# Kernel optimization log

Measured on AMD Instinct MI355X. Metric: run time of the kernel, lower is better.

Reference implementation:

```python
import jax, jax.numpy as jnp
import numpy as np

EMBED = 1024
HEADS = 16
HEAD_DIM = EMBED // HEADS
RANK = 8
ALPHA = 16
SCALE_LORA = ALPHA / RANK  # 2.0


def _lora_linear(x, W, b, A, B):
    # F.linear(x, W, b) + scale * F.linear(F.linear(x, A), B)
    return x @ W.T + b + SCALE_LORA * ((x @ A.T) @ B.T)


def setup_inputs() -> dict:
    key = jax.random.key(0)
    ks = jax.random.split(key, 17)
    d = {"x": jax.random.normal(ks[0], (2, 2048, EMBED), dtype=jnp.float32)}
    names = ["q", "k", "v", "o"]
    i = 1
    for n in names:
        d[f"W{n}"] = jax.random.normal(ks[i], (EMBED, EMBED), dtype=jnp.float32) * 0.02; i += 1
        d[f"b{n}"] = jnp.zeros((EMBED,), dtype=jnp.float32)
        d[f"A{n}"] = jax.random.normal(ks[i], (RANK, EMBED), dtype=jnp.float32) * 0.02; i += 1
        d[f"B{n}"] = jax.random.normal(ks[i], (EMBED, RANK), dtype=jnp.float32) * 0.02; i += 1
    return d


def reference(x, Wq, bq, Aq, Bq, Wk, bk, Ak, Bk, Wv, bv, Av, Bv, Wo, bo, Ao, Bo):
    N, S, _ = x.shape
    Q = _lora_linear(x, Wq, bq, Aq, Bq).reshape(N, S, HEADS, HEAD_DIM)
    K = _lora_linear(x, Wk, bk, Ak, Bk).reshape(N, S, HEADS, HEAD_DIM)
    V = _lora_linear(x, Wv, bv, Av, Bv).reshape(N, S, HEADS, HEAD_DIM)
    # energy: [N, H, Sq, Sk]
    energy = jnp.einsum("nqhd,nkhd->nhqk", Q, K) / jnp.sqrt(jnp.float32(HEAD_DIM))
    attn = jax.nn.softmax(energy, axis=-1)
    out = jnp.einsum("nhqk,nkhd->nqhd", attn, V).reshape(N, S, EMBED)
    return _lora_linear(out, Wo, bo, Ao, Bo)
```

## Files before the change

kernel.cpp:

```cpp
#include <hip/hip_runtime.h>
#include <stdint.h>

typedef uint16_t u16;
typedef short s16x8 __attribute__((ext_vector_type(8)));
typedef float f32x4 __attribute__((ext_vector_type(4)));
typedef unsigned short u16x4 __attribute__((ext_vector_type(4)));
typedef uint32_t u32;
typedef u32 u32x2 __attribute__((ext_vector_type(2)));
typedef u32 u32x4 __attribute__((ext_vector_type(4)));

#define MFMA16(a,b,c) __builtin_amdgcn_mfma_f32_16x16x32_bf16((a),(b),(c),0,0,0)
#define QSCALE 0.18033688011112042f

__device__ __forceinline__ float b2f(u16 b){
  union { u32 u; float f; } v; v.u = ((u32)b)<<16; return v.f;
}
__device__ __forceinline__ u16 f2b(float f){
  union { float f; u32 u; } v; v.f = f;
  return (u16)((v.u + 0x7fffu + ((v.u>>16)&1u))>>16);
}
__device__ __forceinline__ u32 fbits(float f){
  union { float f; u32 u; } v; v.f = f; return v.u;
}
__device__ __forceinline__ void load_lds_16B(const void* g, void* l){
  __builtin_amdgcn_global_load_lds((const __attribute__((address_space(1))) void*)g,
                                   (__attribute__((address_space(3))) void*)l, 16, 0, 0);
}

__global__ __launch_bounds__(256) void conv_kernel(
    const float* __restrict__ x, u16* __restrict__ xb,
    const float* __restrict__ W0, const float* __restrict__ W1,
    const float* __restrict__ W2, const float* __restrict__ W3,
    u16* __restrict__ Wb,
    const float* __restrict__ A0, const float* __restrict__ A1,
    const float* __restrict__ A2, const float* __restrict__ A3,
    u16* __restrict__ Abf)
{
  const int bid = blockIdx.x;
  if (bid < 1024){
    const int g = bid*256 + threadIdx.x;
#pragma unroll
    for (int t=0;t<4;t++){
      const int i4 = g + t*262144;
      const f32x4 v = *(const f32x4*)(x + (size_t)i4*4);
      u16x4 o;
#pragma unroll
      for (int j=0;j<4;j++) o[j] = f2b(v[j]);
      *(u16x4*)(xb + (size_t)i4*4) = o;
    }
    return;
  }
  if (bid < 2048){
    const int cv = bid - 1024;
    const int y = cv>>8;
    const float* src = (y==0)?W0:(y==1)?W1:(y==2)?W2:W3;
    u16* dst = Wb + (size_t)y*1048576;
    const int g = (cv&255)*256 + threadIdx.x;
#pragma unroll
    for (int t=0;t<4;t++){
      const int i4 = g + t*65536;
      const f32x4 v = *(const f32x4*)(src + (size_t)i4*4);
      u16x4 o;
#pragma unroll
      for (int j=0;j<4;j++) o[j] = f2b(v[j]);
      *(u16x4*)(dst + (size_t)i4*4) = o;
    }
    return;
  }
  for (int w = threadIdx.x; w < 8192; w += 256){
    const int proj = w >> 11, rem = w & 2047;
    const int row = rem >> 7, c8 = (rem & 127) << 3;
    u16x4 o0 = u16x4{0,0,0,0}, o1 = u16x4{0,0,0,0};
    if (row < 8){
      const float* ap = ((proj==0)?A0:(proj==1)?A1:(proj==2)?A2:A3) + row*1024 + c8;
      const f32x4 v0 = *(const f32x4*)(ap);
      const f32x4 v1 = *(const f32x4*)(ap+4);
#pragma unroll
      for (int j=0;j<4;j++){ o0[j] = f2b(v0[j]); o1[j] = f2b(v1[j]); }
    }
    u16* dp = Abf + (size_t)(proj*16 + row)*1024 + c8;
    *(u16x4*)(dp)   = o0;
    *(u16x4*)(dp+4) = o1;
  }
}

__global__ __launch_bounds__(256,2) void gemm_qkv_kernel(
    const u16* __restrict__ Xb, const u16* __restrict__ Wb,
    const float* __restrict__ bq, const float* __restrict__ bk, const float* __restrict__ bv,
    const u16* __restrict__ Abf,
    const float* __restrict__ Blq, const float* __restrict__ Blk, const float* __restrict__ Blv,
    u16* __restrict__ Qb, u16* __restrict__ Kb, u16* __restrict__ Vtb)
{
  __shared__ u16 sm[16896];
  u16* AtB = sm;
  u16* BtB = sm + 8192;
  const int tid = threadIdx.x;
  const int wid = tid>>6, lane = tid&63;
  const int quad = lane>>4, l16 = lane&15;
  const int wm = wid>>1, wn = wid&1;
  const int proj = blockIdx.x>>3;
  const int n0 = (blockIdx.x&7)<<7, m0 = blockIdx.y<<7;
  const u16* W = Wb + (size_t)proj*1048576;
  const u16* AbP = Abf + (size_t)proj*16384;
  const float* bias = (proj==0)?bq:(proj==1)?bk:bv;
  const float* Bl   = (proj==0)?Blq:(proj==1)?Blk:Blv;
  const float scale = (proj==0)?QSCALE:1.0f;

  f32x4 acc[4][4];
  f32x4 acc_t[4];
#pragma unroll
  for (int i=0;i<4;i++){
#pragma unroll
    for (int j=0;j<4;j++) acc[i][j] = f32x4{0.f,0.f,0.f,0.f};
    acc_t[i] = f32x4{0.f,0.f,0.f,0.f};
  }

  for (int k0=0;k0<1024;k0+=64){
#pragma unroll
    for (int half=0; half<2; half++){
#pragma unroll
      for (int p=0;p<2;p++){
        const int s = wid*128 + p*64 + lane;
        const int row = s>>2, c = s&3;
        load_lds_16B(Xb + (size_t)(m0+row)*1024 + k0 + half*32 + c*8, AtB + half*4096 + (wid*128+p*64)*8);
        load_lds_16B(W  + (size_t)(n0+row)*1024 + k0 + half*32 + c*8, BtB + half*4096 + (wid*128+p*64)*8);
      }
    }
    __syncthreads();
#pragma unroll
    for (int half=0; half<2; half++){
      s16x8 af[4], bfr[4];
#pragma unroll
      for (int t=0;t<4;t++){
        const int r = wm*64 + t*16 + l16;
        af[t]  = *(const s16x8*)(AtB + half*4096 + r*32 + quad*8);
        const int c = wn*64 + t*16 + l16;
        bfr[t] = *(const s16x8*)(BtB + half*4096 + c*32 + quad*8);
      }
      const s16x8 abf = *(const s16x8*)(AbP + (size_t)l16*1024 + k0 + half*32 + quad*8);
#pragma unroll
      for (int tm=0;tm<4;tm++){
#pragma unroll
        for (int tn=0;tn<4;tn++)
          acc[tm][tn] = MFMA16(af[tm], bfr[tn], acc[tm][tn]);
        acc_t[tm] = MFMA16(af[tm], abf, acc_t[tm]);
      }
    }
    __syncthreads();
  }

  float* tT = (float*)sm;
  if (wn==0 && l16<8){
#pragma unroll
    for (int tm=0;tm<4;tm++)
#pragma unroll
      for (int rg=0;rg<4;rg++)
        tT[(wm*64 + tm*16 + quad*4 + rg)*8 + l16] = acc_t[tm][rg];
  }
  __syncthreads();

  s16x8 tf[4], bfl[4];
#pragma unroll
  for (int t=0;t<4;t++){ tf[t] = s16x8{0,0,0,0,0,0,0,0}; bfl[t] = s16x8{0,0,0,0,0,0,0,0}; }
  if (quad==0){
#pragma unroll
    for (int tm=0;tm<4;tm++){
      const float* tp = tT + (wm*64 + tm*16 + l16)*8;
#pragma unroll
      for (int j=0;j<8;j++) tf[tm][j] = (short)f2b(2.0f*tp[j]);
    }
#pragma unroll
    for (int tn=0;tn<4;tn++){
      const float* bp = Bl + (size_t)(n0 + wn*64 + tn*16 + l16)*8;
      const f32x4 b0 = *(const f32x4*)(bp);
      const f32x4 b1 = *(const f32x4*)(bp+4);
#pragma unroll
      for (int j=0;j<4;j++){ bfl[tn][j] = (short)f2b(b0[j]); bfl[tn][4+j] = (short)f2b(b1[j]); }
    }
  }
#pragma unroll
  for (int tm=0;tm<4;tm++)
#pragma unroll
    for (int tn=0;tn<4;tn++)
      acc[tm][tn] = MFMA16(tf[tm], bfl[tn], acc[tm][tn]);

  if (proj==2){
    __syncthreads();
#pragma unroll
    for (int tn=0;tn<4;tn++){
      const int nl = wn*64 + tn*16 + l16;
      const float bn = bias[n0+nl];
#pragma unroll
      for (int tm=0;tm<4;tm++){
        const int ml = wm*64 + tm*16 + quad*4;
        u16x4 pk;
#pragma unroll
        for (int rg=0;rg<4;rg++) pk[rg] = f2b(acc[tm][tn][rg]+bn);
        *(u16x4*)(sm + nl*132 + ml) = pk;
      }
    }
    __syncthreads();
    const int batch = m0>>11, sbase = m0&2047;
#pragma unroll
    for (int p=0;p<8;p++){
      const int idx = p*256 + tid;
      const int row = idx>>4, c16 = idx&15;
      const s16x8 v = *(const s16x8*)(sm + row*132 + c16*8);
      const int ng = n0 + row, hh = ng>>6, dd = ng&63;
      *(s16x8*)(Vtb + (size_t)((batch*16+hh)*64+dd)*2048 + sbase + c16*8) = v;
    }
  } else {
#pragma unroll
    for (int tn=0;tn<4;tn++){
      const int n = n0 + wn*64 + tn*16 + l16;
      const float bn = bias[n];
#pragma unroll
      for (int tm=0;tm<4;tm++){
        const int mb = m0 + wm*64 + tm*16 + quad*4;
        if (proj==0){
#pragma unroll
          for (int rg=0;rg<4;rg++) Qb[(size_t)(mb+rg)*1024 + n] = f2b((acc[tm][tn][rg]+bn)*scale);
        } else {
#pragma unroll
          for (int rg=0;rg<4;rg++) Kb[(size_t)(mb+rg)*1024 + n] = f2b(acc[tm][tn][rg]+bn);
        }
      }
    }
  }
}

__global__ __launch_bounds__(256,2) void gemm_o_kernel(
    const u16* __restrict__ Xb, const u16* __restrict__ W,
    const float* __restrict__ bias, const u16* __restrict__ Abf,
    const float* __restrict__ Bl, float* __restrict__ Out)
{
  __shared__ u16 At[2][128*32];
  __shared__ u16 Bt[2][64*32];
  const int tid = threadIdx.x;
  const int wid = tid>>6, lane = tid&63;
  const int quad = lane>>4, l16 = lane&15;
  const int wm = wid>>1, wn = wid&1;
  const int m0 = blockIdx.y<<7, n0 = blockIdx.x<<6;
  const u16* AbP = Abf + (size_t)3*16384;

  f32x4 acc[4][2];
  f32x4 acc_t[4];
#pragma unroll
  for (int i=0;i<4;i++){
#pragma unroll
    for (int j=0;j<2;j++) acc[i][j] = f32x4{0.f,0.f,0.f,0.f};
    acc_t[i] = f32x4{0.f,0.f,0.f,0.f};
  }

  for (int k0=0;k0<1024;k0+=64){
#pragma unroll
    for (int half=0; half<2; half++){
#pragma unroll
      for (int p=0;p<2;p++){
        const int s = wid*128 + p*64 + lane;
        const int row = s>>2, c = s&3;
        load_lds_16B(Xb + (size_t)(m0+row)*1024 + k0 + half*32 + c*8, At[half] + (wid*128+p*64)*8);
      }
      { const int s = wid*64 + lane;
        const int row = s>>2, c = s&3;
        load_lds_16B(W + (size_t)(n0+row)*1024 + k0 + half*32 + c*8, Bt[half] + (wid*64)*8); }
    }
    __syncthreads();
#pragma unroll
    for (int half=0; half<2; half++){
      s16x8 af[4], bfr[2];
#pragma unroll
      for (int t=0;t<4;t++){
        const int r = wm*64 + t*16 + l16;
        af[t] = *(const s16x8*)(At[half] + r*32 + quad*8);
      }
#pragma unroll
      for (int t=0;t<2;t++){
        const int c = wn*32 + t*16 + l16;
        bfr[t] = *(const s16x8*)(Bt[half] + c*32 + quad*8);
      }
      const s16x8 abf = *(const s16x8*)(AbP + (size_t)l16*1024 + k0 + half*32 + quad*8);
#pragma unroll
      for (int tm=0;tm<4;tm++){
#pragma unroll
        for (int tn=0;tn<2;tn++)
          acc[tm][tn] = MFMA16(af[tm], bfr[tn], acc[tm][tn]);
        acc_t[tm] = MFMA16(af[tm], abf, acc_t[tm]);
      }
    }
    __syncthreads();
  }

  float* tT = (float*)At;
  if (wn==0 && l16<8){
#pragma unroll
    for (int tm=0;tm<4;tm++)
#pragma unroll
      for (int rg=0;rg<4;rg++)
        tT[(wm*64 + tm*16 + quad*4 + rg)*8 + l16] = acc_t[tm][rg];
  }
  __syncthreads();

  s16x8 tf[4], bfl[2];
#pragma unroll
  for (int t=0;t<4;t++) tf[t] = s16x8{0,0,0,0,0,0,0,0};
#pragma unroll
  for (int t=0;t<2;t++) bfl[t] = s16x8{0,0,0,0,0,0,0,0};
  if (quad==0){
#pragma unroll
    for (int tm=0;tm<4;tm++){
      const float* tp = tT + (wm*64 + tm*16 + l16)*8;
#pragma unroll
      for (int j=0;j<8;j++) tf[tm][j] = (short)f2b(2.0f*tp[j]);
    }
#pragma unroll
    for (int tn=0;tn<2;tn++){
      const float* bp = Bl + (size_t)(n0 + wn*32 + tn*16 + l16)*8;
      const f32x4 b0 = *(const f32x4*)(bp);
      const f32x4 b1 = *(const f32x4*)(bp+4);
#pragma unroll
      for (int j=0;j<4;j++){ bfl[tn][j] = (short)f2b(b0[j]); bfl[tn][4+j] = (short)f2b(b1[j]); }
    }
  }
#pragma unroll
  for (int tm=0;tm<4;tm++)
#pragma unroll
    for (int tn=0;tn<2;tn++)
      acc[tm][tn] = MFMA16(tf[tm], bfl[tn], acc[tm][tn]);

#pragma unroll
  for (int tn=0;tn<2;tn++){
    const int n = n0 + wn*32 + tn*16 + l16;
    const float bn = bias[n];
#pragma unroll
    for (int tm=0;tm<4;tm++){
      const int mb = m0 + wm*64 + tm*16 + quad*4;
#pragma unroll
      for (int rg=0;rg<4;rg++)
        Out[(size_t)(mb+rg)*1024 + n] = acc[tm][tn][rg] + bn;
    }
  }
}

__global__ __launch_bounds__(512,4) void attn_kernel(
    const u16* __restrict__ Q, const u16* __restrict__ K,
    const u16* __restrict__ Vt, u16* __restrict__ Out)
{
  __shared__ u16 KtB[2][128*72];
  __shared__ u16 VtB[2][64*136];
  const int tid = threadIdx.x;
  const int wid = tid>>6, lane = tid&63;
  const int quad = lane>>4, l16 = lane&15;
  const int lin = blockIdx.x + (blockIdx.y<<4) + (blockIdx.z<<8);
  const int swz = (lin&7)*64 + (lin>>3);
  const int q0 = (swz&15)<<7;
  const int h  = (swz>>4)&15;
  const int nb = swz>>8;
  const int qg = wid>>1;
  const int kh = wid&1;
  const int qw = qg*32;

  s16x8 qf[2][2];
#pragma unroll
  for (int g=0;g<2;g++){
    const int row = q0 + qw + g*16 + l16;
#pragma unroll
    for (int dh=0;dh<2;dh++)
      qf[g][dh] = *(const s16x8*)(Q + (size_t)(nb*2048+row)*1024 + h*64 + dh*32 + quad*8);
  }
  f32x4 OT[2][4];
  f32x4 Lacc[2];
#pragma unroll
  for (int g=0;g<2;g++){
#pragma unroll
    for (int td=0;td<4;td++) OT[g][td] = f32x4{0.f,0.f,0.f,0.f};
    Lacc[g] = f32x4{0.f,0.f,0.f,0.f};
  }
  s16x8 ones;
#pragma unroll
  for (int j=0;j<8;j++) ones[j] = (short)0x3F80;

  s16x8 kreg[2], vreg[2];
  auto LOADT = [&](int kn){
#pragma unroll
    for (int p=0;p<2;p++){
      const int s = p*512 + tid;
      kreg[p] = *(const s16x8*)(K + (size_t)(nb*2048+kn+(s>>3))*1024 + h*64 + (s&7)*8);
      vreg[p] = *(const s16x8*)(Vt + (size_t)((nb*16+h)*64+(s>>4))*2048 + kn + (s&15)*8);
    }
  };
  auto WRITET = [&](int b){
    u16* Ktb = KtB[b]; u16* Vtb = VtB[b];
#pragma unroll
    for (int p=0;p<2;p++){
      const int s = p*512 + tid;
      *(s16x8*)(Ktb + (s>>3)*72 + (s&7)*8) = kreg[p];
      *(s16x8*)(Vtb + (s>>4)*136 + (s&15)*8) = vreg[p];
    }
  };

  LOADT(0);
  WRITET(0);
  LOADT(128);
  __syncthreads();

  for (int t=0;t<16;t++){
    const int cur = t&1;
    if (t < 15) WRITET(cur^1);
    if (t < 14) LOADT((t+2)*128);
    const u16* KtC = KtB[cur];
    const u16* VtC = VtB[cur];

#pragma unroll
    for (int kb=0;kb<2;kb++){
      u32 ew[2][2], ow[2][2];
#pragma unroll
      for (int sel=0;sel<2;sel++){
        const int key = kh*64 + kb*32 + sel*16 + l16;
        const s16x8 kf0 = *(const s16x8*)(KtC + key*72 + quad*8);
        const s16x8 kf1 = *(const s16x8*)(KtC + key*72 + 32 + quad*8);
#pragma unroll
        for (int g=0;g<2;g++){
          f32x4 z = f32x4{0.f,0.f,0.f,0.f};
          z = MFMA16(kf0, qf[g][0], z);
          z = MFMA16(kf1, qf[g][1], z);
          const float p0 = __builtin_amdgcn_exp2f(z[0]);
          const float p1 = __builtin_amdgcn_exp2f(z[1]);
          const float p2 = __builtin_amdgcn_exp2f(z[2]);
          const float p3 = __builtin_amdgcn_exp2f(z[3]);
          const u32 w0 = __builtin_amdgcn_perm(fbits(p1), fbits(p0), 0x07060302u);
          const u32 w1 = __builtin_amdgcn_perm(fbits(p3), fbits(p2), 0x07060302u);
          if (sel==0){ ew[g][0]=w0; ew[g][1]=w1; } else { ow[g][0]=w0; ow[g][1]=w1; }
        }
      }
      s16x8 pf[2];
#pragma unroll
      for (int g=0;g<2;g++){
        const u32x2 r32 = __builtin_amdgcn_permlane32_swap(ew[g][0], ow[g][0], false, false);
        const u32x2 r16 = __builtin_amdgcn_permlane16_swap(r32[0], r32[1], false, false);
        const u32x2 s32 = __builtin_amdgcn_permlane32_swap(ew[g][1], ow[g][1], false, false);
        const u32x2 s16v = __builtin_amdgcn_permlane16_swap(s32[0], s32[1], false, false);
        u32x4 pw; pw[0]=r16[0]; pw[1]=s16v[0]; pw[2]=r16[1]; pw[3]=s16v[1];
        pf[g] = __builtin_bit_cast(s16x8, pw);
      }
      __builtin_amdgcn_s_setprio(1);
#pragma unroll
      for (int td=0;td<4;td++){
        const s16x8 vf = *(const s16x8*)(VtC + (td*16+l16)*136 + kh*64 + kb*32 + quad*8);
#pragma unroll
        for (int g=0;g<2;g++)
          OT[g][td] = MFMA16(vf, pf[g], OT[g][td]);
      }
#pragma unroll
      for (int g=0;g<2;g++)
        Lacc[g] = MFMA16(ones, pf[g], Lacc[g]);
      __builtin_amdgcn_s_setprio(0);
    }
    __syncthreads();
  }

  float* ep = (float*)KtB;
  float* lw = (float*)VtB;
  if (kh==1){
#pragma unroll
    for (int g=0;g<2;g++){
      const int q = qw + g*16 + l16;
#pragma unroll
      for (int td=0;td<4;td++)
        *(f32x4*)(ep + q*68 + td*16 + quad*4) = OT[g][td];
      if (quad==0) lw[q] = Lacc[g][0];
    }
  }
  __syncthreads();
  if (kh==0){
#pragma unroll
    for (int g=0;g<2;g++){
      const int q = qw + g*16 + l16;
      const float linv = 1.0f / (Lacc[g][0] + lw[q]);
      const int qout = q0 + q;
#pragma unroll
      for (int td=0;td<4;td++){
        const f32x4 o2 = *(const f32x4*)(ep + q*68 + td*16 + quad*4);
        u16x4 pk;
#pragma unroll
        for (int rg=0;rg<4;rg++) pk[rg] = f2b((OT[g][td][rg]+o2[rg])*linv);
        *(u16x4*)(Out + (size_t)(nb*2048+qout)*1024 + h*64 + td*16 + quad*4) = pk;
      }
    }
  }
}

extern "C" void kernel_launch(void* const* d_in, const int* in_sizes, int n_in,
                              void* d_out, int out_size, void* d_ws, size_t ws_size,
                              hipStream_t stream)
{
  const float* x  = (const float*)d_in[0];
  const float* Wq = (const float*)d_in[1];  const float* bq = (const float*)d_in[2];
  const float* Aq = (const float*)d_in[3];  const float* Bq = (const float*)d_in[4];
  const float* Wk = (const float*)d_in[5];  const float* bk = (const float*)d_in[6];
  const float* Ak = (const float*)d_in[7];  const float* Bk = (const float*)d_in[8];
  const float* Wv = (const float*)d_in[9];  const float* bv = (const float*)d_in[10];
  const float* Av = (const float*)d_in[11]; const float* Bv = (const float*)d_in[12];
  const float* Wo = (const float*)d_in[13]; const float* bo = (const float*)d_in[14];
  const float* Ao = (const float*)d_in[15]; const float* Bo = (const float*)d_in[16];

  char* ws = (char*)d_ws;
  u16* Abf = (u16*)(ws + 0);
  u16* xb  = (u16*)(ws + 524288);
  u16* Ab  = xb;
  u16* Wb  = (u16*)(ws + 524288 + 8388608);
  u16* Qb  = (u16*)(ws + 524288 + 2*8388608);
  u16* Kb  = (u16*)(ws + 524288 + 3*8388608);
  u16* Vtb = (u16*)(ws + 524288 + 4*8388608);

  conv_kernel<<<dim3(2049),256,0,stream>>>(x, xb, Wq, Wk, Wv, Wo, Wb,
                                           Aq, Ak, Av, Ao, Abf);
  gemm_qkv_kernel<<<dim3(24,32),256,0,stream>>>(xb, Wb, bq, bk, bv, Abf,
                                                Bq, Bk, Bv, Qb, Kb, Vtb);
  attn_kernel<<<dim3(16,16,2),512,0,stream>>>(Qb, Kb, Vtb, Ab);
  gemm_o_kernel<<<dim3(16,32),256,0,stream>>>(Ab, Wb + (size_t)3*1048576, bo, Abf, Bo,
                                              (float*)d_out);
}
```

Measured before the change: 220.9 us.

## Read K and V fragments directly from global memory instead of LDS staging

Drops the double-buffered LDS staging of K and transposed V tiles in the attention kernel. Each wave now loads its MFMA operand fragments straight from global memory (relying on L1/L2 caching), and the per-tile __syncthreads is gone. LDS use shrinks to the epilogue reduction buffers. This removes LDS traffic and barriers, but every wave re-fetches K/V from cache with no prefetch overlap, so load latency may be exposed.

```diff
diff --git a/kernel.cpp b/kernel.cpp
--- a/kernel.cpp
+++ b/kernel.cpp
@@ -346,8 +346,8 @@
     const u16* __restrict__ Q, const u16* __restrict__ K,
     const u16* __restrict__ Vt, u16* __restrict__ Out)
 {
-  __shared__ u16 KtB[2][128*72];
-  __shared__ u16 VtB[2][64*136];
+  __shared__ float ep[128*68];
+  __shared__ float lw[128];
   const int tid = threadIdx.x;
   const int wid = tid>>6, lane = tid&63;
   const int quad = lane>>4, l16 = lane&15;
@@ -380,45 +380,21 @@
 #pragma unroll
   for (int j=0;j<8;j++) ones[j] = (short)0x3F80;
 
-  s16x8 kreg[2], vreg[2];
-  auto LOADT = [&](int kn){
-#pragma unroll
-    for (int p=0;p<2;p++){
-      const int s = p*512 + tid;
-      kreg[p] = *(const s16x8*)(K + (size_t)(nb*2048+kn+(s>>3))*1024 + h*64 + (s&7)*8);
-      vreg[p] = *(const s16x8*)(Vt + (size_t)((nb*16+h)*64+(s>>4))*2048 + kn + (s&15)*8);
-    }
-  };
-  auto WRITET = [&](int b){
-    u16* Ktb = KtB[b]; u16* Vtb = VtB[b];
-#pragma unroll
-    for (int p=0;p<2;p++){
-      const int s = p*512 + tid;
-      *(s16x8*)(Ktb + (s>>3)*72 + (s&7)*8) = kreg[p];
-      *(s16x8*)(Vtb + (s>>4)*136 + (s&15)*8) = vreg[p];
-    }
-  };
-
-  LOADT(0);
-  WRITET(0);
-  LOADT(128);
-  __syncthreads();
+  const u16* Kbase  = K  + (size_t)(nb*2048)*1024 + h*64;
+  const u16* Vtbase = Vt + (size_t)((nb*16+h)*64)*2048;
 
   for (int t=0;t<16;t++){
-    const int cur = t&1;
-    if (t < 15) WRITET(cur^1);
-    if (t < 14) LOADT((t+2)*128);
-    const u16* KtC = KtB[cur];
-    const u16* VtC = VtB[cur];
-
+    const int kt = t*128;
 #pragma unroll
     for (int kb=0;kb<2;kb++){
+      const int kcol = kt + kh*64 + kb*32;
       u32 ew[2][2], ow[2][2];
 #pragma unroll
       for (int sel=0;sel<2;sel++){
-        const int key = kh*64 + kb*32 + sel*16 + l16;
-        const s16x8 kf0 = *(const s16x8*)(KtC + key*72 + quad*8);
-        const s16x8 kf1 = *(const s16x8*)(KtC + key*72 + 32 + quad*8);
+        const int key = kcol + sel*16 + l16;
+        const u16* kp = Kbase + (size_t)key*1024 + quad*8;
+        const s16x8 kf0 = *(const s16x8*)(kp);
+        const s16x8 kf1 = *(const s16x8*)(kp + 32);
 #pragma unroll
         for (int g=0;g<2;g++){
           f32x4 z = f32x4{0.f,0.f,0.f,0.f};
@@ -446,7 +422,7 @@
       __builtin_amdgcn_s_setprio(1);
 #pragma unroll
       for (int td=0;td<4;td++){
-        const s16x8 vf = *(const s16x8*)(VtC + (td*16+l16)*136 + kh*64 + kb*32 + quad*8);
+        const s16x8 vf = *(const s16x8*)(Vtbase + (size_t)(td*16+l16)*2048 + kcol + quad*8);
 #pragma unroll
         for (int g=0;g<2;g++)
           OT[g][td] = MFMA16(vf, pf[g], OT[g][td]);
@@ -456,11 +432,8 @@
         Lacc[g] = MFMA16(ones, pf[g], Lacc[g]);
       __builtin_amdgcn_s_setprio(0);
     }
-    __syncthreads();
-  }
-
-  float* ep = (float*)KtB;
-  float* lw = (float*)VtB;
+  }
+
   if (kh==1){
 #pragma unroll
     for (int g=0;g<2;g++){
```

Result: slower. 298.4 us (+35.0%).

## Split O-projection GEMM K dimension across two wave groups with LDS reduction

Applied to the files above, without the earlier changes.

The output projection GEMM now runs 512 threads per block, with two groups of four waves each covering half of the K=1024 reduction. The partial accumulators and LoRA intermediate are summed through shared memory before group 0 runs the epilogue. This doubles the waves available per tile to hide latency in a grid of only 512 blocks. In exchange it adds an LDS reduction with extra barriers, and group 1 sits idle during the epilogue.

```diff
diff --git a/kernel.cpp b/kernel.cpp
--- a/kernel.cpp
+++ b/kernel.cpp
@@ -229,19 +229,24 @@
   }
 }
 
-__global__ __launch_bounds__(256,2) void gemm_o_kernel(
+__global__ __launch_bounds__(512,4) void gemm_o_kernel(
     const u16* __restrict__ Xb, const u16* __restrict__ W,
     const float* __restrict__ bias, const u16* __restrict__ Abf,
     const float* __restrict__ Bl, float* __restrict__ Out)
 {
-  __shared__ u16 At[2][128*32];
-  __shared__ u16 Bt[2][64*32];
+  __shared__ char smem[49152];
   const int tid = threadIdx.x;
   const int wid = tid>>6, lane = tid&63;
   const int quad = lane>>4, l16 = lane&15;
-  const int wm = wid>>1, wn = wid&1;
+  const int kseg = wid>>2;
+  const int w4 = wid&3;
+  const int wm = w4>>1, wn = w4&1;
   const int m0 = blockIdx.y<<7, n0 = blockIdx.x<<6;
   const u16* AbP = Abf + (size_t)3*16384;
+  const int kbase = kseg<<9;
+
+  u16* At = (u16*)smem + kseg*8192;
+  u16* Bt = (u16*)smem + 16384 + kseg*4096;
 
   f32x4 acc[4][2];
   f32x4 acc_t[4];
@@ -252,18 +257,18 @@
     acc_t[i] = f32x4{0.f,0.f,0.f,0.f};
   }
 
-  for (int k0=0;k0<1024;k0+=64){
+  for (int k0=kbase; k0<kbase+512; k0+=64){
 #pragma unroll
     for (int half=0; half<2; half++){
 #pragma unroll
       for (int p=0;p<2;p++){
-        const int s = wid*128 + p*64 + lane;
+        const int s = w4*128 + p*64 + lane;
         const int row = s>>2, c = s&3;
-        load_lds_16B(Xb + (size_t)(m0+row)*1024 + k0 + half*32 + c*8, At[half] + (wid*128+p*64)*8);
-      }
-      { const int s = wid*64 + lane;
+        load_lds_16B(Xb + (size_t)(m0+row)*1024 + k0 + half*32 + c*8, At + half*4096 + (w4*128+p*64)*8);
+      }
+      { const int s = w4*64 + lane;
         const int row = s>>2, c = s&3;
-        load_lds_16B(W + (size_t)(n0+row)*1024 + k0 + half*32 + c*8, Bt[half] + (wid*64)*8); }
+        load_lds_16B(W + (size_t)(n0+row)*1024 + k0 + half*32 + c*8, Bt + half*2048 + (w4*64)*8); }
     }
     __syncthreads();
 #pragma unroll
@@ -272,12 +277,12 @@
 #pragma unroll
       for (int t=0;t<4;t++){
         const int r = wm*64 + t*16 + l16;
-        af[t] = *(const s16x8*)(At[half] + r*32 + quad*8);
+        af[t] = *(const s16x8*)(At + half*4096 + r*32 + quad*8);
       }
 #pragma unroll
       for (int t=0;t<2;t++){
         const int c = wn*32 + t*16 + l16;
-        bfr[t] = *(const s16x8*)(Bt[half] + c*32 + quad*8);
+        bfr[t] = *(const s16x8*)(Bt + half*2048 + c*32 + quad*8);
       }
       const s16x8 abf = *(const s16x8*)(AbP + (size_t)l16*1024 + k0 + half*32 + quad*8);
 #pragma unroll
@@ -291,53 +296,82 @@
     __syncthreads();
   }
 
-  float* tT = (float*)At;
-  if (wn==0 && l16<8){
+  float* ep  = (float*)smem;
+  float* tTp = (float*)(smem + 35072);
+  if (kseg==1){
+#pragma unroll
+    for (int tn=0;tn<2;tn++)
+#pragma unroll
+      for (int tm=0;tm<4;tm++)
+#pragma unroll
+        for (int rg=0;rg<4;rg++)
+          ep[(wm*64+tm*16+quad*4+rg)*68 + wn*32+tn*16+l16] = acc[tm][tn][rg];
+    if (wn==0 && l16<8){
+#pragma unroll
+      for (int tm=0;tm<4;tm++)
+#pragma unroll
+        for (int rg=0;rg<4;rg++)
+          tTp[(wm*64+tm*16+quad*4+rg)*8 + l16] = acc_t[tm][rg];
+    }
+  }
+  __syncthreads();
+  if (kseg==0){
+#pragma unroll
+    for (int tn=0;tn<2;tn++)
+#pragma unroll
+      for (int tm=0;tm<4;tm++)
+#pragma unroll
+        for (int rg=0;rg<4;rg++)
+          acc[tm][tn][rg] += ep[(wm*64+tm*16+quad*4+rg)*68 + wn*32+tn*16+l16];
+    if (wn==0 && l16<8){
+#pragma unroll
+      for (int tm=0;tm<4;tm++)
+#pragma unroll
+        for (int rg=0;rg<4;rg++)
+          tTp[(wm*64+tm*16+quad*4+rg)*8 + l16] += acc_t[tm][rg];
+    }
+  }
+  __syncthreads();
+
+  if (kseg==0){
+    s16x8 tf[4], bfl[2];
+#pragma unroll
+    for (int t=0;t<4;t++) tf[t] = s16x8{0,0,0,0,0,0,0,0};
+#pragma unroll
+    for (int t=0;t<2;t++) bfl[t] = s16x8{0,0,0,0,0,0,0,0};
+    if (quad==0){
+#pragma unroll
+      for (int tm=0;tm<4;tm++){
+        const float* tp = tTp + (wm*64 + tm*16 + l16)*8;
+#pragma unroll
+        for (int j=0;j<8;j++) tf[tm][j] = (short)f2b(2.0f*tp[j]);
+      }
+#pragma unroll
+      for (int tn=0;tn<2;tn++){
+        const float* bp = Bl + (size_t)(n0 + wn*32 + tn*16 + l16)*8;
+        const f32x4 b0 = *(const f32x4*)(bp);
+        const f32x4 b1 = *(const f32x4*)(bp+4);
+#pragma unroll
+        for (int j=0;j<4;j++){ bfl[tn][j] = (short)f2b(b0[j]); bfl[tn][4+j] = (short)f2b(b1[j]); }
+      }
+    }
 #pragma unroll
     for (int tm=0;tm<4;tm++)
 #pragma unroll
-      for (int rg=0;rg<4;rg++)
-        tT[(wm*64 + tm*16 + quad*4 + rg)*8 + l16] = acc_t[tm][rg];
-  }
-  __syncthreads();
-
-  s16x8 tf[4], bfl[2];
-#pragma unroll
-  for (int t=0;t<4;t++) tf[t] = s16x8{0,0,0,0,0,0,0,0};
-#pragma unroll
-  for (int t=0;t<2;t++) bfl[t] = s16x8{0,0,0,0,0,0,0,0};
-  if (quad==0){
-#pragma unroll
-    for (int tm=0;tm<4;tm++){
-      const float* tp = tT + (wm*64 + tm*16 + l16)*8;
-#pragma unroll
-      for (int j=0;j<8;j++) tf[tm][j] = (short)f2b(2.0f*tp[j]);
-    }
+      for (int tn=0;tn<2;tn++)
+        acc[tm][tn] = MFMA16(tf[tm], bfl[tn], acc[tm][tn]);
+
 #pragma unroll
     for (int tn=0;tn<2;tn++){
-      const float* bp = Bl + (size_t)(n0 + wn*32 + tn*16 + l16)*8;
-      const f32x4 b0 = *(const f32x4*)(bp);
-      const f32x4 b1 = *(const f32x4*)(bp+4);
-#pragma unroll
-      for (int j=0;j<4;j++){ bfl[tn][j] = (short)f2b(b0[j]); bfl[tn][4+j] = (short)f2b(b1[j]); }
-    }
-  }
-#pragma unroll
-  for (int tm=0;tm<4;tm++)
-#pragma unroll
-    for (int tn=0;tn<2;tn++)
-      acc[tm][tn] = MFMA16(tf[tm], bfl[tn], acc[tm][tn]);
-
-#pragma unroll
-  for (int tn=0;tn<2;tn++){
-    const int n = n0 + wn*32 + tn*16 + l16;
-    const float bn = bias[n];
-#pragma unroll
-    for (int tm=0;tm<4;tm++){
-      const int mb = m0 + wm*64 + tm*16 + quad*4;
-#pragma unroll
-      for (int rg=0;rg<4;rg++)
-        Out[(size_t)(mb+rg)*1024 + n] = acc[tm][tn][rg] + bn;
+      const int n = n0 + wn*32 + tn*16 + l16;
+      const float bn = bias[n];
+#pragma unroll
+      for (int tm=0;tm<4;tm++){
+        const int mb = m0 + wm*64 + tm*16 + quad*4;
+#pragma unroll
+        for (int rg=0;rg<4;rg++)
+          Out[(size_t)(mb+rg)*1024 + n] = acc[tm][tn][rg] + bn;
+      }
     }
   }
 }
@@ -518,6 +552,6 @@
   gemm_qkv_kernel<<<dim3(24,32),256,0,stream>>>(xb, Wb, bq, bk, bv, Abf,
                                                 Bq, Bk, Bv, Qb, Kb, Vtb);
   attn_kernel<<<dim3(16,16,2),512,0,stream>>>(Qb, Kb, Vtb, Ab);
-  gemm_o_kernel<<<dim3(16,32),256,0,stream>>>(Ab, Wb + (size_t)3*1048576, bo, Abf, Bo,
+  gemm_o_kernel<<<dim3(16,32),512,0,stream>>>(Ab, Wb + (size_t)3*1048576, bo, Abf, Bo,
                                               (float*)d_out);
 }
```

New measurement: 216.8 us. No clear change (-1.9%).
